# Kernel optimization log

Hardware: AMD Instinct MI355X
Metric: run time of the kernel (lower is better)

Reference implementation:

```python
import jax, jax.numpy as jnp
import numpy as np

B, N, F_IN, HID, OUT, NHEADS = 16, 1024, 64, 64, 64, 4
TAXI = 512        # get_Parameter('taxi_size') from the original repo (node split point)
ALPHA = 0.2       # LeakyReLU negative slope


def setup_inputs() -> dict:
    key = jax.random.key(0)
    ks = jax.random.split(key, 8)
    x = jax.random.normal(ks[0], (B, N, F_IN), dtype=jnp.float32)
    # multiplicative binary mask (mostly ones so softmax rows are well-conditioned)
    mask = (jax.random.uniform(ks[1], (N, N)) > 0.1).astype(jnp.float32)
    s_in = 1.0 / np.sqrt(F_IN)
    s_cat = 1.0 / np.sqrt(NHEADS * HID)
    W1 = jax.random.normal(ks[2], (NHEADS, F_IN, HID), jnp.float32) * s_in
    W2 = jax.random.normal(ks[3], (NHEADS, F_IN, HID), jnp.float32) * s_in
    a = jax.random.normal(ks[4], (NHEADS, 2 * HID), jnp.float32) * 0.1
    W1o = jax.random.normal(ks[5], (NHEADS * HID, OUT), jnp.float32) * s_cat
    W2o = jax.random.normal(ks[6], (NHEADS * HID, OUT), jnp.float32) * s_cat
    ao = jax.random.normal(ks[7], (2 * OUT,), jnp.float32) * 0.1
    return dict(x=x, mask=mask, W1=W1, W2=W2, a=a, W1o=W1o, W2o=W2o, ao=ao)


def _gat_layer(x, mask, W1, W2, a, out_dim):
    # x: [B,N,F]; W1,W2: [F,out_dim]; a: [2*out_dim]
    # node-group-split linear projection (taxi nodes via W1, rest via W2)
    h = jnp.concatenate([x[:, :TAXI] @ W1, x[:, TAXI:] @ W2], axis=1)  # [B,N,O]
    A1 = h @ a[:out_dim]                 # [B,N]
    A2 = h @ a[out_dim:]                 # [B,N]
    sim = A1[:, :, None] + A2[:, None, :]  # [B,N,N] additive scores
    e = jax.nn.leaky_relu(sim, ALPHA)
    e = mask[None, :, :] * e             # multiplicative mask (as in source)
    attn = jax.nn.softmax(e, axis=-1)    # [B,N,N]  (dropout omitted: eval mode)
    h_prime = jnp.einsum('bnm,bmo->bno', attn, h)
    return jax.nn.elu(h_prime), attn


def reference(x, mask, W1, W2, a, W1o, W2o, ao):
    # input dropout omitted (eval mode)
    heads = [_gat_layer(x, mask, W1[i], W2[i], a[i], HID)[0] for i in range(NHEADS)]
    xc = jnp.concatenate(heads, axis=-1)          # [B,N,NHEADS*HID]
    out, attn = _gat_layer(xc, mask, W1o, W2o, ao, OUT)
    return out, attn
```

## Files before the change

### kernel.cpp

```cpp
#include <hip/hip_runtime.h>
#include <hip/hip_bf16.h>

#define B_      16
#define N_      1024
#define ALPHA_  0.2f

typedef __attribute__((ext_vector_type(8))) __bf16 bf16x8;
typedef __attribute__((ext_vector_type(4))) float  floatx4;

__device__ __forceinline__ float eluf(float u) { return u > 0.f ? u : __expf(u) - 1.f; }

__device__ __forceinline__ floatx4 mfma_bf16(bf16x8 a, bf16x8 b, floatx4 c) {
    return __builtin_amdgcn_mfma_f32_16x16x32_bf16(a, b, c, 0, 0, 0);
}

__global__ __launch_bounds__(256) void maskbits_kernel(
    const float* __restrict__ mask, unsigned* __restrict__ bits)
{
    const int idx = blockIdx.x * 256 + threadIdx.x;
    const float* src = mask + (size_t)idx * 32;
    unsigned v = 0;
#pragma unroll
    for (int j = 0; j < 8; ++j) {
        float4 f = *(const float4*)(src + j * 4);
        v |= ((unsigned)(f.x != 0.f)) << (j * 4 + 0);
        v |= ((unsigned)(f.y != 0.f)) << (j * 4 + 1);
        v |= ((unsigned)(f.z != 0.f)) << (j * 4 + 2);
        v |= ((unsigned)(f.w != 0.f)) << (j * 4 + 3);
    }
    bits[idx] = v;
}

__global__ __launch_bounds__(256) void proj1_kernel(
    const float* __restrict__ x, const float* __restrict__ W1,
    const float* __restrict__ W2, const float* __restrict__ av,
    __bf16* __restrict__ h1t, float* __restrict__ A1, float* __restrict__ A2)
{
    const int tile = blockIdx.x, b = blockIdx.y, head = blockIdx.z;
    const int n0 = tile * 64;
    const float* W  = ((n0 < 512) ? W1 : W2) + head * 64 * 64;
    const float* ah = av + head * 128;

    __shared__ __align__(16) __bf16 xs[64][72];
    __shared__ __align__(16) __bf16 Wt[64][72];
    __shared__ __align__(16) float as_[128];

    const int tid = threadIdx.x;
    if (tid < 128) as_[tid] = ah[tid];
#pragma unroll
    for (int i = 0; i < 4; ++i) {
        int idx = i * 256 + tid;
        int r = idx >> 4, c = (idx & 15) * 4;
        float4 v = *(const float4*)(x + ((size_t)(b * N_ + n0 + r)) * 64 + c);
        xs[r][c+0] = (__bf16)v.x; xs[r][c+1] = (__bf16)v.y;
        xs[r][c+2] = (__bf16)v.z; xs[r][c+3] = (__bf16)v.w;
        float4 wv = *(const float4*)(W + (size_t)r * 64 + c);
        Wt[c+0][r] = (__bf16)wv.x; Wt[c+1][r] = (__bf16)wv.y;
        Wt[c+2][r] = (__bf16)wv.z; Wt[c+3][r] = (__bf16)wv.w;
    }
    __syncthreads();

    const int w = tid >> 6, L = tid & 63, quad = L >> 4, lo = L & 15;
    floatx4 acc[4] = {{0,0,0,0},{0,0,0,0},{0,0,0,0},{0,0,0,0}};
#pragma unroll
    for (int kc = 0; kc < 2; ++kc) {
        bf16x8 af = *(bf16x8*)&xs[16 * w + lo][kc * 32 + quad * 8];
#pragma unroll
        for (int t = 0; t < 4; ++t) {
            bf16x8 bv = *(bf16x8*)&Wt[16 * t + lo][kc * 32 + quad * 8];
            acc[t] = mfma_bf16(af, bv, acc[t]);
        }
    }

    float p1[4] = {0, 0, 0, 0}, p2[4] = {0, 0, 0, 0};
#pragma unroll
    for (int t = 0; t < 4; ++t) {
        float a1w = as_[16 * t + lo], a2w = as_[64 + 16 * t + lo];
#pragma unroll
        for (int i = 0; i < 4; ++i) { p1[i] += acc[t][i] * a1w; p2[i] += acc[t][i] * a2w; }
    }
#pragma unroll
    for (int s = 1; s < 16; s <<= 1)
#pragma unroll
        for (int i = 0; i < 4; ++i) {
            p1[i] += __shfl_xor(p1[i], s);
            p2[i] += __shfl_xor(p2[i], s);
        }
    const int bh = head * B_ + b;
    if (lo == 0) {
#pragma unroll
        for (int i = 0; i < 4; ++i) {
            int n = 16 * w + quad * 4 + i;
            A1[bh * N_ + n0 + n] = p1[i];
            A2[bh * N_ + n0 + n] = p2[i];
        }
    }

    __syncthreads();
#pragma unroll
    for (int t = 0; t < 4; ++t)
#pragma unroll
        for (int i = 0; i < 4; ++i)
            xs[16 * w + quad * 4 + i][16 * t + lo] = (__bf16)acc[t][i];
    __syncthreads();
    const int d = tid & 63, ch = tid >> 6;
    bf16x8 v0, v1;
#pragma unroll
    for (int j = 0; j < 8; ++j) v0[j] = xs[ch * 16 + j][d];
#pragma unroll
    for (int j = 0; j < 8; ++j) v1[j] = xs[ch * 16 + 8 + j][d];
    bf16x8* dst = (bf16x8*)(h1t + ((size_t)bh * 64 + d) * N_ + n0 + ch * 16);
    dst[0] = v0; dst[1] = v1;
}

__global__ __launch_bounds__(256, 4) void attn1_kernel(
    const float* __restrict__ A1g, const float* __restrict__ A2g,
    const __bf16* __restrict__ Htg, const unsigned* __restrict__ bitsG,
    __bf16* __restrict__ xc_out)
{
    const int b = blockIdx.x, head = blockIdx.y, tile = blockIdx.z;
    const int n0 = tile * 64;
    const int bh = head * B_ + b;
    const float* A2 = A2g + (size_t)bh * N_;
    const __bf16* Hglob = Htg + (size_t)bh * 64 * N_;

    __shared__ __align__(16) __bf16 ts[64][72];
    __shared__ __align__(16) __bf16 Ht[64][72];
    __shared__ __align__(16) float A2s[N_];
    __shared__ __align__(16) unsigned bitsS[2048];
    __shared__ float invz[64];

    const int tid = threadIdx.x;
    *(float4*)&A2s[tid * 4] = *(const float4*)(A2 + tid * 4);
    {
        uint4 u0 = *(const uint4*)(bitsG + n0 * 32 + tid * 8);
        uint4 u1 = *(const uint4*)(bitsG + n0 * 32 + tid * 8 + 4);
        const int row = tid >> 2, wb0 = (tid & 3) * 8;
        bitsS[(wb0+0)*64+row] = u0.x; bitsS[(wb0+1)*64+row] = u0.y;
        bitsS[(wb0+2)*64+row] = u0.z; bitsS[(wb0+3)*64+row] = u0.w;
        bitsS[(wb0+4)*64+row] = u1.x; bitsS[(wb0+5)*64+row] = u1.y;
        bitsS[(wb0+6)*64+row] = u1.z; bitsS[(wb0+7)*64+row] = u1.w;
    }

    const int r = tid >> 2, q = tid & 3;
    const float a1r = A1g[(size_t)bh * N_ + n0 + r];
    const int w = tid >> 6, L = tid & 63, quad = L >> 4, lo = L & 15;
    const __bf16* hrow = Hglob + (size_t)r * N_ + q * 16;

    floatx4 acc[4] = {{0,0,0,0},{0,0,0,0},{0,0,0,0},{0,0,0,0}};
    float zacc = 0.f;

    for (int mt = 0; mt < 16; ++mt) {
        __syncthreads();
        bf16x8 h0 = *(const bf16x8*)(hrow + mt * 64);
        bf16x8 h1 = *(const bf16x8*)(hrow + mt * 64 + 8);
        const int mb = mt * 64 + q * 16;
        const unsigned wb = bitsS[(mt * 2 + (q >> 1)) * 64 + r] >> ((q & 1) * 16);
        float o[16];
#pragma unroll
        for (int j = 0; j < 16; ++j) {
            float s = a1r + A2s[mb + j];
            float lr = fmaxf(s, ALPHA_ * s);
            float t = ((wb >> j) & 1u) ? __expf(lr) : 1.f;
            zacc += t; o[j] = t;
        }
        bf16x8 pk0 = {(__bf16)o[0], (__bf16)o[1], (__bf16)o[2], (__bf16)o[3],
                      (__bf16)o[4], (__bf16)o[5], (__bf16)o[6], (__bf16)o[7]};
        bf16x8 pk1 = {(__bf16)o[8], (__bf16)o[9], (__bf16)o[10], (__bf16)o[11],
                      (__bf16)o[12], (__bf16)o[13], (__bf16)o[14], (__bf16)o[15]};
        *(bf16x8*)&ts[r][q * 16]     = pk0;
        *(bf16x8*)&ts[r][q * 16 + 8] = pk1;
        *(bf16x8*)&Ht[r][q * 16]     = h0;
        *(bf16x8*)&Ht[r][q * 16 + 8] = h1;
        __syncthreads();
#pragma unroll
        for (int c = 0; c < 2; ++c) {
            bf16x8 af = *(bf16x8*)&ts[16 * w + lo][c * 32 + quad * 8];
#pragma unroll
            for (int t = 0; t < 4; ++t) {
                bf16x8 bv = *(bf16x8*)&Ht[16 * t + lo][c * 32 + quad * 8];
                acc[t] = mfma_bf16(af, bv, acc[t]);
            }
        }
    }

    zacc += __shfl_xor(zacc, 1);
    zacc += __shfl_xor(zacc, 2);
    if (q == 0) invz[r] = 1.f / zacc;
    __syncthreads();

#pragma unroll
    for (int t = 0; t < 4; ++t)
#pragma unroll
        for (int i = 0; i < 4; ++i) {
            const int n = 16 * w + quad * 4 + i;
            ts[n][16 * t + lo] = (__bf16)eluf(acc[t][i] * invz[n]);
        }
    __syncthreads();
#pragma unroll
    for (int i = 0; i < 2; ++i) {
        int cid = i * 256 + tid;
        int row = cid >> 3, c8 = (cid & 7) * 8;
        bf16x8 v = *(bf16x8*)&ts[row][c8];
        *(bf16x8*)(xc_out + ((size_t)(b * N_ + n0 + row)) * 256 + head * 64 + c8) = v;
    }
}

__global__ __launch_bounds__(256) void attn2_kernel(
    const float* __restrict__ A1g, const float* __restrict__ A2g,
    const __bf16* __restrict__ Htg, const unsigned* __restrict__ bitsG,
    float* __restrict__ out_f, float* __restrict__ attn_f)
{
    const int b = blockIdx.x, tile = blockIdx.z;
    const int n0 = tile * 32;
    const float* A2 = A2g + (size_t)b * N_;
    const __bf16* Hglob = Htg + (size_t)b * 64 * N_;

    __shared__ __align__(16) __bf16 ts[32][72];
    __shared__ __align__(16) __bf16 Ht[64][72];
    __shared__ __align__(16) float A2s[N_];
    __shared__ __align__(16) unsigned bitsS[1024];
    __shared__ float invz[32];

    const int tid = threadIdx.x;
    *(float4*)&A2s[tid * 4] = *(const float4*)(A2 + tid * 4);
    {
        uint4 u = *(const uint4*)(bitsG + n0 * 32 + tid * 4);
        const int row = tid >> 3, wb0 = (tid & 7) * 4;
        bitsS[(wb0+0)*32+row] = u.x; bitsS[(wb0+1)*32+row] = u.y;
        bitsS[(wb0+2)*32+row] = u.z; bitsS[(wb0+3)*32+row] = u.w;
    }

    const int r2 = tid >> 3, q2 = tid & 7;
    const float a1r = A1g[(size_t)b * N_ + n0 + r2];
    const int dr = tid >> 2, dq = tid & 3;
    const int w = tid >> 6, L = tid & 63, quad = L >> 4, lo = L & 15;
    const __bf16* hrow = Hglob + (size_t)dr * N_ + dq * 16;

    floatx4 acc2[2] = {{0,0,0,0},{0,0,0,0}};
    float zacc = 0.f;
    bf16x8 tr[16];

    for (int mt = 0; mt < 16; ++mt) {
        __syncthreads();
        bf16x8 h0 = *(const bf16x8*)(hrow + mt * 64);
        bf16x8 h1 = *(const bf16x8*)(hrow + mt * 64 + 8);
        const int mb = mt * 64 + q2 * 8;
        const unsigned wb = bitsS[(mt * 2 + (q2 >> 2)) * 32 + r2] >> ((q2 & 3) * 8);
        float o[8];
#pragma unroll
        for (int j = 0; j < 8; ++j) {
            float s = a1r + A2s[mb + j];
            float lr = fmaxf(s, ALPHA_ * s);
            float t = ((wb >> j) & 1u) ? __expf(lr) : 1.f;
            zacc += t; o[j] = t;
        }
        bf16x8 pk = {(__bf16)o[0], (__bf16)o[1], (__bf16)o[2], (__bf16)o[3],
                     (__bf16)o[4], (__bf16)o[5], (__bf16)o[6], (__bf16)o[7]};
        tr[mt] = pk;
        *(bf16x8*)&ts[r2][q2 * 8] = pk;
        *(bf16x8*)&Ht[dr][dq * 16]     = h0;
        *(bf16x8*)&Ht[dr][dq * 16 + 8] = h1;
        __syncthreads();
#pragma unroll
        for (int c = 0; c < 2; ++c) {
#pragma unroll
            for (int rt = 0; rt < 2; ++rt) {
                bf16x8 af = *(bf16x8*)&ts[16 * rt + lo][c * 32 + quad * 8];
                bf16x8 bv = *(bf16x8*)&Ht[16 * w + lo][c * 32 + quad * 8];
                acc2[rt] = mfma_bf16(af, bv, acc2[rt]);
            }
        }
    }

    zacc += __shfl_xor(zacc, 1);
    zacc += __shfl_xor(zacc, 2);
    zacc += __shfl_xor(zacc, 4);
    if (q2 == 0) invz[r2] = 1.f / zacc;
    __syncthreads();

#pragma unroll
    for (int rt = 0; rt < 2; ++rt)
#pragma unroll
        for (int i = 0; i < 4; ++i) {
            const int n = 16 * rt + quad * 4 + i;
            out_f[((size_t)(b * N_ + n0 + n)) * 64 + 16 * w + lo] =
                eluf(acc2[rt][i] * invz[n]);
        }

    const float iz = invz[r2];
    float* arow = attn_f + ((size_t)(b * N_ + n0 + r2)) * N_ + q2 * 8;
#pragma unroll
    for (int mt = 0; mt < 16; ++mt) {
        bf16x8 t8 = tr[mt];
        float4 f0 = make_float4((float)t8[0] * iz, (float)t8[1] * iz,
                                (float)t8[2] * iz, (float)t8[3] * iz);
        float4 f1 = make_float4((float)t8[4] * iz, (float)t8[5] * iz,
                                (float)t8[6] * iz, (float)t8[7] * iz);
        *(float4*)(arow + mt * 64)     = f0;
        *(float4*)(arow + mt * 64 + 4) = f1;
    }
}

__global__ __launch_bounds__(256) void proj2_kernel(
    const __bf16* __restrict__ xcb, const float* __restrict__ W1o,
    const float* __restrict__ W2o, const float* __restrict__ ao,
    __bf16* __restrict__ h2t, float* __restrict__ A1o, float* __restrict__ A2o)
{
    const int tile = blockIdx.x, b = blockIdx.y;
    const int n0 = tile * 64;
    const float* W = (n0 < 512) ? W1o : W2o;

    __shared__ __align__(16) __bf16 xs[64][264];
    __shared__ __align__(16) __bf16 Wt[64][264];
    __shared__ __align__(16) float as_[128];

    const int tid = threadIdx.x;
    if (tid < 128) as_[tid] = ao[tid];

#pragma unroll
    for (int i = 0; i < 8; ++i) {
        int idx = i * 256 + tid;
        int row = idx >> 5, c = (idx & 31) * 8;
        *(bf16x8*)&xs[row][c] =
            *(const bf16x8*)(xcb + ((size_t)(b * N_ + n0 + row)) * 256 + c);
    }
#pragma unroll
    for (int i = 0; i < 16; ++i) {
        int idx = i * 256 + tid;
        int k = idx >> 4, n4 = (idx & 15) * 4;
        float4 wv = *(const float4*)(W + (size_t)k * 64 + n4);
        Wt[n4 + 0][k] = (__bf16)wv.x;
        Wt[n4 + 1][k] = (__bf16)wv.y;
        Wt[n4 + 2][k] = (__bf16)wv.z;
        Wt[n4 + 3][k] = (__bf16)wv.w;
    }
    __syncthreads();

    const int w = tid >> 6, L = tid & 63, quad = L >> 4, lo = L & 15;
    floatx4 acc[4] = {{0,0,0,0},{0,0,0,0},{0,0,0,0},{0,0,0,0}};
#pragma unroll
    for (int kc = 0; kc < 8; ++kc) {
        bf16x8 af = *(bf16x8*)&xs[16 * w + lo][kc * 32 + quad * 8];
#pragma unroll
        for (int t = 0; t < 4; ++t) {
            bf16x8 bv = *(bf16x8*)&Wt[16 * t + lo][kc * 32 + quad * 8];
            acc[t] = mfma_bf16(af, bv, acc[t]);
        }
    }

    float p1[4] = {0, 0, 0, 0}, p2[4] = {0, 0, 0, 0};
#pragma unroll
    for (int t = 0; t < 4; ++t) {
        float a1w = as_[16 * t + lo], a2w = as_[64 + 16 * t + lo];
#pragma unroll
        for (int i = 0; i < 4; ++i) { p1[i] += acc[t][i] * a1w; p2[i] += acc[t][i] * a2w; }
    }
#pragma unroll
    for (int s = 1; s < 16; s <<= 1)
#pragma unroll
        for (int i = 0; i < 4; ++i) {
            p1[i] += __shfl_xor(p1[i], s);
            p2[i] += __shfl_xor(p2[i], s);
        }
    if (lo == 0) {
#pragma unroll
        for (int i = 0; i < 4; ++i) {
            int n = 16 * w + quad * 4 + i;
            A1o[b * N_ + n0 + n] = p1[i];
            A2o[b * N_ + n0 + n] = p2[i];
        }
    }

    __syncthreads();
#pragma unroll
    for (int t = 0; t < 4; ++t)
#pragma unroll
        for (int i = 0; i < 4; ++i)
            xs[16 * w + quad * 4 + i][16 * t + lo] = (__bf16)acc[t][i];
    __syncthreads();
    const int d = tid & 63, ch = tid >> 6;
    bf16x8 v0, v1;
#pragma unroll
    for (int j = 0; j < 8; ++j) v0[j] = xs[ch * 16 + j][d];
#pragma unroll
    for (int j = 0; j < 8; ++j) v1[j] = xs[ch * 16 + 8 + j][d];
    bf16x8* dst = (bf16x8*)(h2t + ((size_t)b * 64 + d) * N_ + n0 + ch * 16);
    dst[0] = v0; dst[1] = v1;
}

extern "C" void kernel_launch(void* const* d_in, const int* in_sizes, int n_in,
                              void* d_out, int out_size, void* d_ws, size_t ws_size,
                              hipStream_t stream)
{
    const float* x    = (const float*)d_in[0];
    const float* mask = (const float*)d_in[1];
    const float* W1   = (const float*)d_in[2];
    const float* W2   = (const float*)d_in[3];
    const float* a    = (const float*)d_in[4];
    const float* W1o  = (const float*)d_in[5];
    const float* W2o  = (const float*)d_in[6];
    const float* ao   = (const float*)d_in[7];

    float* out      = (float*)d_out;
    float* attn_out = out + (size_t)B_ * N_ * 64;

    float*    ws    = (float*)d_ws;
    float*    A1    = ws;
    float*    A2    = A1 + 65536;
    float*    A1o   = A2 + 65536;
    float*    A2o   = A1o + 16384;
    __bf16*   h1t   = (__bf16*)(A2o + 16384);
    __bf16*   h2t   = h1t + 4194304;
    __bf16*   xcb   = h2t + 1048576;
    unsigned* bitsG = (unsigned*)(xcb + 4194304);

    maskbits_kernel<<<dim3(128), 256, 0, stream>>>(mask, bitsG);
    proj1_kernel<<<dim3(16, 16, 4), 256, 0, stream>>>(x, W1, W2, a, h1t, A1, A2);
    attn1_kernel<<<dim3(16, 4, 16), 256, 0, stream>>>(A1, A2, h1t, bitsG, xcb);
    proj2_kernel<<<dim3(16, 16, 1), 256, 0, stream>>>(xcb, W1o, W2o, ao, h2t, A1o, A2o);
    attn2_kernel<<<dim3(16, 1, 32), 256, 0, stream>>>(A1o, A2o, h2t, bitsG, out, attn_out);
}
```

Measured before the change: 157.6 us.

## Double-buffer H tiles and compute scores in MFMA register layout

In attn1, each lane now computes the softmax numerators directly in the MFMA A-operand layout. This removes the ts shared-memory round trip for scores. H tiles are double-buffered in LDS with the next tile prefetched from global, so each iteration needs one barrier instead of two. attn2 gets similar double buffering for both the score and H tiles, with the next tile's scores computed before the current MFMAs. Both kernels swap the masked-exp branch for a bitmask AND before expf and use vectorized A2 loads; the cost is more LDS per block, which may lower occupancy.

```diff
diff --git a/kernel.cpp b/kernel.cpp
--- a/kernel.cpp
+++ b/kernel.cpp
@@ -124,11 +124,10 @@
     const float* A2 = A2g + (size_t)bh * N_;
     const __bf16* Hglob = Htg + (size_t)bh * 64 * N_;
 
+    __shared__ __align__(16) __bf16 Ht[2][64][72];
     __shared__ __align__(16) __bf16 ts[64][72];
-    __shared__ __align__(16) __bf16 Ht[64][72];
     __shared__ __align__(16) float A2s[N_];
     __shared__ __align__(16) unsigned bitsS[2048];
-    __shared__ float invz[64];
 
     const int tid = threadIdx.x;
     *(float4*)&A2s[tid * 4] = *(const float4*)(A2 + tid * 4);
@@ -142,60 +141,79 @@
         bitsS[(wb0+6)*64+row] = u1.z; bitsS[(wb0+7)*64+row] = u1.w;
     }
 
-    const int r = tid >> 2, q = tid & 3;
-    const float a1r = A1g[(size_t)bh * N_ + n0 + r];
+    const int sr = tid >> 2, sq = tid & 3;
+    const __bf16* hrow = Hglob + (size_t)sr * N_ + sq * 16;
     const int w = tid >> 6, L = tid & 63, quad = L >> 4, lo = L & 15;
-    const __bf16* hrow = Hglob + (size_t)r * N_ + q * 16;
+    const int nloc = 16 * w + lo;
+    const float a1r = A1g[(size_t)bh * N_ + n0 + nloc];
+    const int shq = quad * 8;
+
+    bf16x8 h0 = *(const bf16x8*)(hrow);
+    bf16x8 h1 = *(const bf16x8*)(hrow + 8);
+    *(bf16x8*)&Ht[0][sr][sq * 16]     = h0;
+    *(bf16x8*)&Ht[0][sr][sq * 16 + 8] = h1;
+    __syncthreads();
 
     floatx4 acc[4] = {{0,0,0,0},{0,0,0,0},{0,0,0,0},{0,0,0,0}};
     float zacc = 0.f;
 
     for (int mt = 0; mt < 16; ++mt) {
-        __syncthreads();
-        bf16x8 h0 = *(const bf16x8*)(hrow + mt * 64);
-        bf16x8 h1 = *(const bf16x8*)(hrow + mt * 64 + 8);
-        const int mb = mt * 64 + q * 16;
-        const unsigned wb = bitsS[(mt * 2 + (q >> 1)) * 64 + r] >> ((q & 1) * 16);
-        float o[16];
-#pragma unroll
-        for (int j = 0; j < 16; ++j) {
-            float s = a1r + A2s[mb + j];
-            float lr = fmaxf(s, ALPHA_ * s);
-            float t = ((wb >> j) & 1u) ? __expf(lr) : 1.f;
-            zacc += t; o[j] = t;
-        }
-        bf16x8 pk0 = {(__bf16)o[0], (__bf16)o[1], (__bf16)o[2], (__bf16)o[3],
-                      (__bf16)o[4], (__bf16)o[5], (__bf16)o[6], (__bf16)o[7]};
-        bf16x8 pk1 = {(__bf16)o[8], (__bf16)o[9], (__bf16)o[10], (__bf16)o[11],
-                      (__bf16)o[12], (__bf16)o[13], (__bf16)o[14], (__bf16)o[15]};
-        *(bf16x8*)&ts[r][q * 16]     = pk0;
-        *(bf16x8*)&ts[r][q * 16 + 8] = pk1;
-        *(bf16x8*)&Ht[r][q * 16]     = h0;
-        *(bf16x8*)&Ht[r][q * 16 + 8] = h1;
-        __syncthreads();
-#pragma unroll
-        for (int c = 0; c < 2; ++c) {
-            bf16x8 af = *(bf16x8*)&ts[16 * w + lo][c * 32 + quad * 8];
-#pragma unroll
-            for (int t = 0; t < 4; ++t) {
-                bf16x8 bv = *(bf16x8*)&Ht[16 * t + lo][c * 32 + quad * 8];
-                acc[t] = mfma_bf16(af, bv, acc[t]);
+        const int cur = mt & 1;
+        if (mt < 15) {
+            h0 = *(const bf16x8*)(hrow + (mt + 1) * 64);
+            h1 = *(const bf16x8*)(hrow + (mt + 1) * 64 + 8);
+        }
+        bf16x8 pf0, pf1;
+#pragma unroll
+        for (int kc = 0; kc < 2; ++kc) {
+            const int mb = mt * 64 + kc * 32 + shq;
+            const unsigned wbk = bitsS[(mt * 2 + kc) * 64 + nloc] >> shq;
+            float4 alo = *(const float4*)&A2s[mb];
+            float4 ahi = *(const float4*)&A2s[mb + 4];
+            float a2v[8] = {alo.x, alo.y, alo.z, alo.w, ahi.x, ahi.y, ahi.z, ahi.w};
+            float o[8];
+#pragma unroll
+            for (int j = 0; j < 8; ++j) {
+                float s = a1r + a2v[j];
+                float lr = fmaxf(s, ALPHA_ * s);
+                int bm = (int)(wbk << (31 - j)) >> 31;
+                lr = __int_as_float(__float_as_int(lr) & bm);
+                float t = __expf(lr);
+                zacc += t; o[j] = t;
             }
-        }
-    }
-
-    zacc += __shfl_xor(zacc, 1);
-    zacc += __shfl_xor(zacc, 2);
-    if (q == 0) invz[r] = 1.f / zacc;
-    __syncthreads();
+            bf16x8 pk = {(__bf16)o[0], (__bf16)o[1], (__bf16)o[2], (__bf16)o[3],
+                         (__bf16)o[4], (__bf16)o[5], (__bf16)o[6], (__bf16)o[7]};
+            if (kc == 0) pf0 = pk; else pf1 = pk;
+        }
+#pragma unroll
+        for (int t = 0; t < 4; ++t) {
+            bf16x8 bv = *(bf16x8*)&Ht[cur][16 * t + lo][shq];
+            acc[t] = mfma_bf16(pf0, bv, acc[t]);
+        }
+#pragma unroll
+        for (int t = 0; t < 4; ++t) {
+            bf16x8 bv = *(bf16x8*)&Ht[cur][16 * t + lo][32 + shq];
+            acc[t] = mfma_bf16(pf1, bv, acc[t]);
+        }
+        if (mt < 15) {
+            *(bf16x8*)&Ht[cur ^ 1][sr][sq * 16]     = h0;
+            *(bf16x8*)&Ht[cur ^ 1][sr][sq * 16 + 8] = h1;
+            __syncthreads();
+        }
+    }
+
+    zacc += __shfl_xor(zacc, 16);
+    zacc += __shfl_xor(zacc, 32);
+    const float invz = 1.f / zacc;
+    float iz[4];
+#pragma unroll
+    for (int i = 0; i < 4; ++i) iz[i] = __shfl(invz, quad * 4 + i);
 
 #pragma unroll
     for (int t = 0; t < 4; ++t)
 #pragma unroll
-        for (int i = 0; i < 4; ++i) {
-            const int n = 16 * w + quad * 4 + i;
-            ts[n][16 * t + lo] = (__bf16)eluf(acc[t][i] * invz[n]);
-        }
+        for (int i = 0; i < 4; ++i)
+            ts[16 * w + quad * 4 + i][16 * t + lo] = (__bf16)eluf(acc[t][i] * iz[i]);
     __syncthreads();
 #pragma unroll
     for (int i = 0; i < 2; ++i) {
@@ -216,8 +234,8 @@
     const float* A2 = A2g + (size_t)b * N_;
     const __bf16* Hglob = Htg + (size_t)b * 64 * N_;
 
-    __shared__ __align__(16) __bf16 ts[32][72];
-    __shared__ __align__(16) __bf16 Ht[64][72];
+    __shared__ __align__(16) __bf16 ts2[2][32][72];
+    __shared__ __align__(16) __bf16 Ht2[2][64][72];
     __shared__ __align__(16) float A2s[N_];
     __shared__ __align__(16) unsigned bitsS[1024];
     __shared__ float invz[32];
@@ -241,35 +259,63 @@
     float zacc = 0.f;
     bf16x8 tr[16];
 
-    for (int mt = 0; mt < 16; ++mt) {
-        __syncthreads();
-        bf16x8 h0 = *(const bf16x8*)(hrow + mt * 64);
-        bf16x8 h1 = *(const bf16x8*)(hrow + mt * 64 + 8);
+    __syncthreads();
+
+    auto scores = [&](int mt) -> bf16x8 {
         const int mb = mt * 64 + q2 * 8;
         const unsigned wb = bitsS[(mt * 2 + (q2 >> 2)) * 32 + r2] >> ((q2 & 3) * 8);
+        float4 alo = *(const float4*)&A2s[mb];
+        float4 ahi = *(const float4*)&A2s[mb + 4];
+        float a2v[8] = {alo.x, alo.y, alo.z, alo.w, ahi.x, ahi.y, ahi.z, ahi.w};
         float o[8];
 #pragma unroll
         for (int j = 0; j < 8; ++j) {
-            float s = a1r + A2s[mb + j];
+            float s = a1r + a2v[j];
             float lr = fmaxf(s, ALPHA_ * s);
-            float t = ((wb >> j) & 1u) ? __expf(lr) : 1.f;
+            int bm = (int)(wb << (31 - j)) >> 31;
+            lr = __int_as_float(__float_as_int(lr) & bm);
+            float t = __expf(lr);
             zacc += t; o[j] = t;
         }
         bf16x8 pk = {(__bf16)o[0], (__bf16)o[1], (__bf16)o[2], (__bf16)o[3],
                      (__bf16)o[4], (__bf16)o[5], (__bf16)o[6], (__bf16)o[7]};
-        tr[mt] = pk;
-        *(bf16x8*)&ts[r2][q2 * 8] = pk;
-        *(bf16x8*)&Ht[dr][dq * 16]     = h0;
-        *(bf16x8*)&Ht[dr][dq * 16 + 8] = h1;
-        __syncthreads();
-#pragma unroll
-        for (int c = 0; c < 2; ++c) {
+        return pk;
+    };
+
+    {
+        bf16x8 h0 = *(const bf16x8*)(hrow);
+        bf16x8 h1 = *(const bf16x8*)(hrow + 8);
+        bf16x8 pk = scores(0);
+        tr[0] = pk;
+        *(bf16x8*)&ts2[0][r2][q2 * 8]      = pk;
+        *(bf16x8*)&Ht2[0][dr][dq * 16]     = h0;
+        *(bf16x8*)&Ht2[0][dr][dq * 16 + 8] = h1;
+    }
+    __syncthreads();
+
+#pragma unroll
+    for (int mt = 0; mt < 16; ++mt) {
+        const int cur = mt & 1;
+        bf16x8 h0, h1, pk;
+        if (mt < 15) {
+            h0 = *(const bf16x8*)(hrow + (mt + 1) * 64);
+            h1 = *(const bf16x8*)(hrow + (mt + 1) * 64 + 8);
+            pk = scores(mt + 1);
+            tr[mt + 1] = pk;
+        }
+#pragma unroll
+        for (int c = 0; c < 2; ++c)
 #pragma unroll
             for (int rt = 0; rt < 2; ++rt) {
-                bf16x8 af = *(bf16x8*)&ts[16 * rt + lo][c * 32 + quad * 8];
-                bf16x8 bv = *(bf16x8*)&Ht[16 * w + lo][c * 32 + quad * 8];
+                bf16x8 af = *(bf16x8*)&ts2[cur][16 * rt + lo][c * 32 + quad * 8];
+                bf16x8 bv = *(bf16x8*)&Ht2[cur][16 * w + lo][c * 32 + quad * 8];
                 acc2[rt] = mfma_bf16(af, bv, acc2[rt]);
             }
+        if (mt < 15) {
+            *(bf16x8*)&ts2[cur ^ 1][r2][q2 * 8]      = pk;
+            *(bf16x8*)&Ht2[cur ^ 1][dr][dq * 16]     = h0;
+            *(bf16x8*)&Ht2[cur ^ 1][dr][dq * 16 + 8] = h1;
+            __syncthreads();
         }
     }
 
```

Result: faster. 153.8 us (-2.4%).
